# Performance work log

Hardware: AMD Instinct MI355X
Metric: run time of the kernel (lower is better)

## Reference

```python
import jax, jax.numpy as jnp
import numpy as np

N_NODES = 10000
N_EDGES = 500000
IN_DIM = 512
HID = 256
VOCAB = 1000


def _gat(x, src, dst, W, a_src, a_dst, b, n):
    # PyG GATConv, heads=1: linear, per-edge attention logits,
    # segment softmax over target node, scatter-weighted-sum.
    h = x @ W                              # [N, C]
    e = jax.nn.leaky_relu(jnp.take(h @ a_src, src) + jnp.take(h @ a_dst, dst), 0.2)  # [E]
    m = jax.ops.segment_max(e, dst, num_segments=n)
    w = jnp.exp(e - m[dst])
    denom = jax.ops.segment_sum(w, dst, num_segments=n)
    alpha = w / denom[dst]                 # [E]
    out = jax.ops.segment_sum(alpha[:, None] * h[src], dst, num_segments=n)  # [N, C]
    return out + b


def _lstm(seq, W_ih, W_hh, b_ih, b_hh):
    # torch nn.LSTM single layer, gate order i,f,g,o; batch of 1 -> scan over nodes
    H = W_hh.shape[1]
    pre = seq @ W_ih.T + (b_ih + b_hh)     # [T, 4H] precomputed input projection

    def step(carry, xt):
        h, c = carry
        g = xt + h @ W_hh.T
        i, f, gg, o = jnp.split(g, 4)
        i = jax.nn.sigmoid(i); f = jax.nn.sigmoid(f)
        gg = jnp.tanh(gg); o = jax.nn.sigmoid(o)
        c = f * c + i * gg
        h = o * jnp.tanh(c)
        return (h, c), h

    init = (jnp.zeros((H,), seq.dtype), jnp.zeros((H,), seq.dtype))
    _, hs = jax.lax.scan(step, init, pre)
    return hs                               # [T, H]


def setup_inputs() -> dict:
    key = jax.random.key(0)
    ks = jax.random.split(key, 16)
    s = 0.05
    x = jax.random.normal(ks[0], (N_NODES, IN_DIM), jnp.float32)
    edge_index = jax.random.randint(ks[1], (2, N_EDGES), 0, N_NODES, jnp.int32)
    return {
        "x": x,
        "W1": jax.random.normal(ks[2], (IN_DIM, HID), jnp.float32) * s,
        "a_src1": jax.random.normal(ks[3], (HID,), jnp.float32) * s,
        "a_dst1": jax.random.normal(ks[4], (HID,), jnp.float32) * s,
        "b1": jnp.zeros((HID,), jnp.float32),
        "W2": jax.random.normal(ks[5], (HID, HID), jnp.float32) * s,
        "a_src2": jax.random.normal(ks[6], (HID,), jnp.float32) * s,
        "a_dst2": jax.random.normal(ks[7], (HID,), jnp.float32) * s,
        "b2": jnp.zeros((HID,), jnp.float32),
        "W_ih": jax.random.normal(ks[8], (4 * HID, HID), jnp.float32) * s,
        "W_hh": jax.random.normal(ks[9], (4 * HID, HID), jnp.float32) * s,
        "b_ih": jnp.zeros((4 * HID,), jnp.float32),
        "b_hh": jnp.zeros((4 * HID,), jnp.float32),
        "Wfc": jax.random.normal(ks[10], (VOCAB, HID), jnp.float32) * s,
        "bfc": jnp.zeros((VOCAB,), jnp.float32),
        "edge_index": edge_index,
    }


def reference(x, W1, a_src1, a_dst1, b1, W2, a_src2, a_dst2, b2,
              W_ih, W_hh, b_ih, b_hh, Wfc, bfc, edge_index):
    n = x.shape[0]
    loops = jnp.arange(n, dtype=edge_index.dtype)
    src = jnp.concatenate([edge_index[0], loops])  # PyG adds self-loops
    dst = jnp.concatenate([edge_index[1], loops])
    h = jax.nn.relu(_gat(x, src, dst, W1, a_src1, a_dst1, b1, n))
    h = _gat(h, src, dst, W2, a_src2, a_dst2, b2, n)
    hs = _lstm(h, W_ih, W_hh, b_ih, b_hh)          # [N, HID]
    logits = hs @ Wfc.T + bfc                      # [N, VOCAB]
    return logits
```

## Files before the change

### kernel.cpp

```cpp
#include <hip/hip_runtime.h>
#include <cstdint>

#define N_NODES 10000
#define N_EDGES 500000
#define E_TOT   510000
#define IN_DIM  512
#define HID     256
#define VOCAB   1000

typedef _Float16 h2v __attribute__((ext_vector_type(2)));

__device__ __forceinline__ float fdot2f(h2v a, h2v b, float c) {
#if __has_builtin(__builtin_amdgcn_fdot2)
    return __builtin_amdgcn_fdot2(a, b, c, false);
#else
    return c + (float)a[0] * (float)b[0] + (float)a[1] * (float)b[1];
#endif
}

__device__ __forceinline__ float sigmoidf_(float x) {
    return 1.f / (1.f + __expf(-x));
}
__device__ __forceinline__ float tanhf_(float x) {
    float ax = fabsf(x);
    float e  = __expf(-2.f * ax);
    float r  = (1.f - e) / (1.f + e);
    return x < 0.f ? -r : r;
}

__device__ __forceinline__ unsigned uc4(const uint4& v, int j) {
    return j == 0 ? v.x : j == 1 ? v.y : j == 2 ? v.z : v.w;
}
__device__ __forceinline__ h2v bch(unsigned u) {
    return __builtin_bit_cast(h2v, u);
}
__device__ __forceinline__ h2v packf2(float2 v) {
    h2v w; w[0] = (_Float16)v.x; w[1] = (_Float16)v.y; return w;
}

template<bool TRANSB, int EPI>
__global__ __launch_bounds__(256) void gemm64(
    const float* __restrict__ A, const float* __restrict__ B,
    const float* __restrict__ bias, const float* __restrict__ bias2,
    float* __restrict__ C, int M, int N, int K, int ldc)
{
    __shared__ float As[16][68];
    __shared__ float Bs[16][68];
    const int tid = threadIdx.x;
    const int tx = tid & 15, ty = tid >> 4;
    const int m0 = blockIdx.x * 64, n0 = blockIdx.y * 64;
    float acc[4][4] = {};

    for (int k0 = 0; k0 < K; k0 += 16) {
        {
            int row = tid >> 2, col = (tid & 3) << 2;
            float4 v = make_float4(0.f, 0.f, 0.f, 0.f);
            if (m0 + row < M)
                v = *(const float4*)(A + (size_t)(m0 + row) * K + k0 + col);
            As[col + 0][row] = v.x; As[col + 1][row] = v.y;
            As[col + 2][row] = v.z; As[col + 3][row] = v.w;
        }
        if (!TRANSB) {
            int row = tid >> 4, col = (tid & 15) << 2;
            const float* bp = B + (size_t)(k0 + row) * N + n0 + col;
            float4 v = make_float4(0.f, 0.f, 0.f, 0.f);
            if (n0 + col + 3 < N) v = *(const float4*)bp;
            else {
                if (n0 + col + 0 < N) v.x = bp[0];
                if (n0 + col + 1 < N) v.y = bp[1];
                if (n0 + col + 2 < N) v.z = bp[2];
            }
            *(float4*)&Bs[row][col] = v;
        } else {
            int nr = tid >> 2, kc = (tid & 3) << 2;
            float4 v = make_float4(0.f, 0.f, 0.f, 0.f);
            if (n0 + nr < N)
                v = *(const float4*)(B + (size_t)(n0 + nr) * K + k0 + kc);
            Bs[kc + 0][nr] = v.x; Bs[kc + 1][nr] = v.y;
            Bs[kc + 2][nr] = v.z; Bs[kc + 3][nr] = v.w;
        }
        __syncthreads();
        #pragma unroll
        for (int kk = 0; kk < 16; ++kk) {
            float a[4], b[4];
            *(float4*)a = *(const float4*)&As[kk][ty << 2];
            *(float4*)b = *(const float4*)&Bs[kk][tx << 2];
            #pragma unroll
            for (int i = 0; i < 4; ++i)
                #pragma unroll
                for (int j = 0; j < 4; ++j)
                    acc[i][j] = fmaf(a[i], b[j], acc[i][j]);
        }
        __syncthreads();
    }
    #pragma unroll
    for (int i = 0; i < 4; ++i) {
        int m = m0 + (ty << 2) + i;
        if (m >= M) continue;
        #pragma unroll
        for (int j = 0; j < 4; ++j) {
            int n = n0 + (tx << 2) + j;
            if (n >= N) continue;
            float v = acc[i][j];
            if (bias)  v += bias[n];
            if (bias2) v += bias2[n];
            if (EPI == 1)
                C[(size_t)m * ldc + (((n & 255) << 2) + (n >> 8))] = v;
            else
                C[(size_t)m * ldc + n] = v;
        }
    }
}

__global__ __launch_bounds__(256) void scores_kernel(
    const float* __restrict__ H, const float* __restrict__ asrc,
    const float* __restrict__ adst, float* __restrict__ ssrc,
    float* __restrict__ sdst)
{
    int node = blockIdx.x * 4 + (threadIdx.x >> 6);
    int lane = threadIdx.x & 63;
    if (node >= N_NODES) return;
    float4 h = ((const float4*)H)[node * 64 + lane];
    float4 a = ((const float4*)asrc)[lane];
    float4 b = ((const float4*)adst)[lane];
    float ps = h.x * a.x + h.y * a.y + h.z * a.z + h.w * a.w;
    float pd = h.x * b.x + h.y * b.y + h.z * b.z + h.w * b.w;
    #pragma unroll
    for (int off = 32; off > 0; off >>= 1) {
        ps += __shfl_xor(ps, off);
        pd += __shfl_xor(pd, off);
    }
    if (lane == 0) { ssrc[node] = ps; sdst[node] = pd; }
}

__global__ __launch_bounds__(256) void edge_w_kernel(
    const int* __restrict__ ei, const float* __restrict__ ssrc,
    const float* __restrict__ sdst, float* __restrict__ wbuf,
    float* __restrict__ denom)
{
    int e = blockIdx.x * 256 + threadIdx.x;
    if (e >= E_TOT) return;
    int s, d;
    if (e < N_EDGES) { s = ei[e]; d = ei[N_EDGES + e]; }
    else             { s = d = e - N_EDGES; }
    float v = ssrc[s] + sdst[d];
    v = (v > 0.f) ? v : 0.2f * v;
    float w = __expf(v);
    wbuf[e] = w;
    unsafeAtomicAdd(&denom[d], w);
}

__global__ __launch_bounds__(256) void scatter_kernel(
    const int* __restrict__ ei, const float* __restrict__ H,
    const float* __restrict__ wbuf, float* __restrict__ S)
{
    int e = blockIdx.x * 4 + (threadIdx.x >> 6);
    int lane = threadIdx.x & 63;
    if (e >= E_TOT) return;
    int s, d;
    if (e < N_EDGES) { s = ei[e]; d = ei[N_EDGES + e]; }
    else             { s = d = e - N_EDGES; }
    float w = wbuf[e];
    float4 h = ((const float4*)H)[s * 64 + lane];
    float* outp = S + (size_t)d * HID + lane * 4;
    unsafeAtomicAdd(outp + 0, w * h.x);
    unsafeAtomicAdd(outp + 1, w * h.y);
    unsafeAtomicAdd(outp + 2, w * h.z);
    unsafeAtomicAdd(outp + 3, w * h.w);
}

__global__ __launch_bounds__(256) void finalize_kernel(
    const float* __restrict__ S, const float* __restrict__ denom,
    const float* __restrict__ bias, float* __restrict__ H, int relu)
{
    int idx = blockIdx.x * 256 + threadIdx.x;
    int n = idx >> 8, ci = idx & 255;
    float v = S[idx] / denom[n] + bias[ci];
    if (relu) v = fmaxf(v, 0.f);
    H[idx] = v;
}

__global__ __launch_bounds__(512, 2) void lstm_kernel(
    const float* __restrict__ Whh,
    const float* __restrict__ pre4,
    float* __restrict__ hs,
    uint4* __restrict__ oL2,
    int T)
{
    __shared__ uint4  oLds[512 * 8];
    __shared__ uint4  hsh[32];
    __shared__ float4 pf4[512];

    const int t  = threadIdx.x;
    const int r0 = t & 255, s = t >> 8;
    const int sw = t & 7;
    const int t8 = t * 8;

    h2v wi[64], wf[64], wg[64];
    {
        const float2* Wr = (const float2*)(Whh + (size_t)r0 * 256 + s * 128);
        #pragma unroll
        for (int j = 0; j < 64; ++j) wi[j] = packf2(Wr[j]);
        Wr = (const float2*)(Whh + (size_t)(r0 + 256) * 256 + s * 128);
        #pragma unroll
        for (int j = 0; j < 64; ++j) wf[j] = packf2(Wr[j]);
        Wr = (const float2*)(Whh + (size_t)(r0 + 512) * 256 + s * 128);
        #pragma unroll
        for (int j = 0; j < 64; ++j) wg[j] = packf2(Wr[j]);
        const float2* Wo = (const float2*)(Whh + (size_t)(r0 + 768) * 256 + s * 128);
        #pragma unroll
        for (int q = 0; q < 16; ++q) {
            unsigned dd[4];
            #pragma unroll
            for (int p = 0; p < 4; ++p)
                dd[p] = __builtin_bit_cast(unsigned, packf2(Wo[q * 4 + p]));
            uint4 pk = make_uint4(dd[0], dd[1], dd[2], dd[3]);
            if (q < 8) oLds[t8 + (q ^ sw)] = pk;
            else       oL2[(q - 8) * 512 + t] = pk;
        }
    }
    if (t < 32) hsh[t] = make_uint4(0, 0, 0, 0);
    float c = 0.f;
    float4 pren = make_float4(0.f, 0.f, 0.f, 0.f);
    if (t < 256) pren = ((const float4*)pre4)[t];
    __syncthreads();

    for (int step = 0; step < T; ++step) {
        float4 pnxt = pren;
        if (t < 256) {
            int ni = (step + 1 < T) ? (step + 1) : step;
            pnxt = ((const float4*)pre4)[(size_t)ni * 256 + t];
        }
        float ai, af, ag, ao;
        if (t < 256) { ai = pren.x; af = pren.y; ag = pren.z; ao = pren.w; }
        else         { ai = 0.f;    af = 0.f;    ag = 0.f;    ao = 0.f;    }

        #pragma unroll
        for (int ch = 0; ch < 8; ++ch) {
            uint4 ha = hsh[s * 16 + ch * 2 + 0];
            uint4 hb = hsh[s * 16 + ch * 2 + 1];
            uint4 oa, ob;
            if (ch < 4) {
                oa = oLds[t8 + ((2 * ch + 0) ^ sw)];
                ob = oLds[t8 + ((2 * ch + 1) ^ sw)];
            } else {
                oa = oL2[(size_t)(2 * ch - 8) * 512 + t];
                ob = oL2[(size_t)(2 * ch - 7) * 512 + t];
            }
            #pragma unroll
            for (int j = 0; j < 4; ++j) {
                h2v hh = bch(uc4(ha, j));
                ai = fdot2f(wi[ch * 8 + j], hh, ai);
                af = fdot2f(wf[ch * 8 + j], hh, af);
                ag = fdot2f(wg[ch * 8 + j], hh, ag);
                ao = fdot2f(bch(uc4(oa, j)), hh, ao);
            }
            #pragma unroll
            for (int j = 0; j < 4; ++j) {
                h2v hh = bch(uc4(hb, j));
                ai = fdot2f(wi[ch * 8 + 4 + j], hh, ai);
                af = fdot2f(wf[ch * 8 + 4 + j], hh, af);
                ag = fdot2f(wg[ch * 8 + 4 + j], hh, ag);
                ao = fdot2f(bch(uc4(ob, j)), hh, ao);
            }
        }
        pf4[t] = make_float4(ai, af, ag, ao);
        __syncthreads();
        if (t < 256) {
            float4 p0 = pf4[t], p1 = pf4[t + 256];
            float i_ = sigmoidf_(p0.x + p1.x);
            float f_ = sigmoidf_(p0.y + p1.y);
            float g_ = tanhf_(p0.z + p1.z);
            float o_ = sigmoidf_(p0.w + p1.w);
            c = fmaf(f_, c, i_ * g_);
            float hv = o_ * tanhf_(c);
            hs[(size_t)step * HID + t] = hv;
            ((_Float16*)hsh)[t] = (_Float16)hv;
            pren = pnxt;
        }
        __syncthreads();
    }
}

extern "C" void kernel_launch(void* const* d_in, const int* in_sizes, int n_in,
                              void* d_out, int out_size, void* d_ws, size_t ws_size,
                              hipStream_t stream)
{
    const float* x   = (const float*)d_in[0];
    const float* W1  = (const float*)d_in[1];
    const float* as1 = (const float*)d_in[2];
    const float* ad1 = (const float*)d_in[3];
    const float* b1  = (const float*)d_in[4];
    const float* W2  = (const float*)d_in[5];
    const float* as2 = (const float*)d_in[6];
    const float* ad2 = (const float*)d_in[7];
    const float* b2  = (const float*)d_in[8];
    const float* Wih = (const float*)d_in[9];
    const float* Whh = (const float*)d_in[10];
    const float* bih = (const float*)d_in[11];
    const float* bhh = (const float*)d_in[12];
    const float* Wfc = (const float*)d_in[13];
    const float* bfc = (const float*)d_in[14];
    const int*   ei  = (const int*)d_in[15];
    float* out = (float*)d_out;

    float* ws    = (float*)d_ws;
    float* A     = ws;
    float* Bsc   = ws +  2560000;
    float* Cbuf  = ws +  5120000;
    float* pre   = ws +  7680000;
    float* wbuf  = ws + 17920000;
    float* denom = ws + 18430000;
    float* ssrc  = ws + 18440000;
    float* sdst  = ws + 18450000;

    dim3 blk(256);

    gemm64<false, 0><<<dim3(157, 4), blk, 0, stream>>>(
        x, W1, nullptr, nullptr, A, N_NODES, HID, IN_DIM, HID);
    scores_kernel<<<2500, blk, 0, stream>>>(A, as1, ad1, ssrc, sdst);
    hipMemsetAsync(Bsc, 0, (size_t)N_NODES * HID * 4, stream);
    hipMemsetAsync(denom, 0, (size_t)N_NODES * 4, stream);
    edge_w_kernel<<<(E_TOT + 255) / 256, blk, 0, stream>>>(ei, ssrc, sdst, wbuf, denom);
    scatter_kernel<<<E_TOT / 4, blk, 0, stream>>>(ei, A, wbuf, Bsc);
    finalize_kernel<<<N_NODES, blk, 0, stream>>>(Bsc, denom, b1, Cbuf, 1);

    gemm64<false, 0><<<dim3(157, 4), blk, 0, stream>>>(
        Cbuf, W2, nullptr, nullptr, A, N_NODES, HID, HID, HID);
    scores_kernel<<<2500, blk, 0, stream>>>(A, as2, ad2, ssrc, sdst);
    hipMemsetAsync(Bsc, 0, (size_t)N_NODES * HID * 4, stream);
    hipMemsetAsync(denom, 0, (size_t)N_NODES * 4, stream);
    edge_w_kernel<<<(E_TOT + 255) / 256, blk, 0, stream>>>(ei, ssrc, sdst, wbuf, denom);
    scatter_kernel<<<E_TOT / 4, blk, 0, stream>>>(ei, A, wbuf, Bsc);
    finalize_kernel<<<N_NODES, blk, 0, stream>>>(Bsc, denom, b2, Cbuf, 0);

    gemm64<true, 1><<<dim3(157, 16), blk, 0, stream>>>(
        Cbuf, Wih, bih, bhh, pre, N_NODES, 4 * HID, HID, 4 * HID);
    lstm_kernel<<<1, 512, 0, stream>>>(Whh, pre, A, (uint4*)Bsc, N_NODES);

    gemm64<true, 0><<<dim3(157, 16), blk, 0, stream>>>(
        A, Wfc, bfc, nullptr, out, N_NODES, VOCAB, HID, VOCAB);
}
```

Measured before the change: 21.62 ms.

## Pair adjacent lanes per LSTM row, reduce via shuffle, double-buffer hidden state

Each LSTM hidden row is now split across two adjacent lanes, so the two partial sums are combined with a shuffle instead of an LDS exchange. This removes one of the two block barriers per timestep. The hidden state is double-buffered in LDS so the next step's h can be written without a second sync. The o-gate weights are redistributed: part stays in registers and the rest goes to LDS, which removes the global-memory (L2) spill of those weights at the cost of higher register pressure.

```diff
diff --git a/kernel.cpp b/kernel.cpp
--- a/kernel.cpp
+++ b/kernel.cpp
@@ -184,100 +184,85 @@
     const float* __restrict__ Whh,
     const float* __restrict__ pre4,
     float* __restrict__ hs,
-    uint4* __restrict__ oL2,
     int T)
 {
-    __shared__ uint4  oLds[512 * 8];
-    __shared__ uint4  hsh[32];
-    __shared__ float4 pf4[512];
+    __shared__ uint4 oT[12 * 512];
+    __shared__ uint4 hbuf[2][32];
 
     const int t  = threadIdx.x;
-    const int r0 = t & 255, s = t >> 8;
-    const int sw = t & 7;
-    const int t8 = t * 8;
-
-    h2v wi[64], wf[64], wg[64];
+    const int r  = t >> 1;
+    const int s  = t & 1;
+    const int hb = s << 4;
+
+    h2v wi[64], wf[64], wg[64], wo[16];
     {
-        const float2* Wr = (const float2*)(Whh + (size_t)r0 * 256 + s * 128);
+        const float2* Wr = (const float2*)(Whh + (size_t)r * 256 + s * 128);
         #pragma unroll
         for (int j = 0; j < 64; ++j) wi[j] = packf2(Wr[j]);
-        Wr = (const float2*)(Whh + (size_t)(r0 + 256) * 256 + s * 128);
+        Wr = (const float2*)(Whh + (size_t)(r + 256) * 256 + s * 128);
         #pragma unroll
         for (int j = 0; j < 64; ++j) wf[j] = packf2(Wr[j]);
-        Wr = (const float2*)(Whh + (size_t)(r0 + 512) * 256 + s * 128);
+        Wr = (const float2*)(Whh + (size_t)(r + 512) * 256 + s * 128);
         #pragma unroll
         for (int j = 0; j < 64; ++j) wg[j] = packf2(Wr[j]);
-        const float2* Wo = (const float2*)(Whh + (size_t)(r0 + 768) * 256 + s * 128);
-        #pragma unroll
-        for (int q = 0; q < 16; ++q) {
+        const float2* Wo = (const float2*)(Whh + (size_t)(r + 768) * 256 + s * 128);
+        #pragma unroll
+        for (int j = 0; j < 16; ++j) wo[j] = packf2(Wo[j]);
+        #pragma unroll
+        for (int k = 0; k < 12; ++k) {
             unsigned dd[4];
             #pragma unroll
             for (int p = 0; p < 4; ++p)
-                dd[p] = __builtin_bit_cast(unsigned, packf2(Wo[q * 4 + p]));
-            uint4 pk = make_uint4(dd[0], dd[1], dd[2], dd[3]);
-            if (q < 8) oLds[t8 + (q ^ sw)] = pk;
-            else       oL2[(q - 8) * 512 + t] = pk;
-        }
-    }
-    if (t < 32) hsh[t] = make_uint4(0, 0, 0, 0);
+                dd[p] = __builtin_bit_cast(unsigned, packf2(Wo[16 + k * 4 + p]));
+            oT[k * 512 + t] = make_uint4(dd[0], dd[1], dd[2], dd[3]);
+        }
+    }
+    if (t < 32) { hbuf[0][t] = make_uint4(0, 0, 0, 0); }
     float c = 0.f;
-    float4 pren = make_float4(0.f, 0.f, 0.f, 0.f);
-    if (t < 256) pren = ((const float4*)pre4)[t];
+    float4 pren = ((const float4*)pre4)[r];
     __syncthreads();
 
     for (int step = 0; step < T; ++step) {
-        float4 pnxt = pren;
-        if (t < 256) {
-            int ni = (step + 1 < T) ? (step + 1) : step;
-            pnxt = ((const float4*)pre4)[(size_t)ni * 256 + t];
-        }
+        const uint4* hcur = hbuf[step & 1];
+        uint4*       hnxt = hbuf[(step + 1) & 1];
+
+        int ni = (step + 1 < T) ? (step + 1) : step;
+        float4 pnxt = ((const float4*)pre4)[(size_t)ni * 256 + r];
+
         float ai, af, ag, ao;
-        if (t < 256) { ai = pren.x; af = pren.y; ag = pren.z; ao = pren.w; }
-        else         { ai = 0.f;    af = 0.f;    ag = 0.f;    ao = 0.f;    }
-
-        #pragma unroll
-        for (int ch = 0; ch < 8; ++ch) {
-            uint4 ha = hsh[s * 16 + ch * 2 + 0];
-            uint4 hb = hsh[s * 16 + ch * 2 + 1];
-            uint4 oa, ob;
-            if (ch < 4) {
-                oa = oLds[t8 + ((2 * ch + 0) ^ sw)];
-                ob = oLds[t8 + ((2 * ch + 1) ^ sw)];
-            } else {
-                oa = oL2[(size_t)(2 * ch - 8) * 512 + t];
-                ob = oL2[(size_t)(2 * ch - 7) * 512 + t];
-            }
+        if (s == 0) { ai = pren.x; af = pren.y; ag = pren.z; ao = pren.w; }
+        else        { ai = 0.f;    af = 0.f;    ag = 0.f;    ao = 0.f;    }
+
+        #pragma unroll
+        for (int k = 0; k < 16; ++k) {
+            uint4 hk = hcur[hb + k];
+            uint4 ok = (k < 4) ? __builtin_bit_cast(uint4, *(const h2v(*)[4])&wo[k * 4])
+                               : oT[(k - 4) * 512 + t];
             #pragma unroll
             for (int j = 0; j < 4; ++j) {
-                h2v hh = bch(uc4(ha, j));
-                ai = fdot2f(wi[ch * 8 + j], hh, ai);
-                af = fdot2f(wf[ch * 8 + j], hh, af);
-                ag = fdot2f(wg[ch * 8 + j], hh, ag);
-                ao = fdot2f(bch(uc4(oa, j)), hh, ao);
+                h2v hh = bch(uc4(hk, j));
+                ai = fdot2f(wi[k * 4 + j], hh, ai);
+                af = fdot2f(wf[k * 4 + j], hh, af);
+                ag = fdot2f(wg[k * 4 + j], hh, ag);
+                ao = fdot2f(bch(uc4(ok, j)), hh, ao);
             }
-            #pragma unroll
-            for (int j = 0; j < 4; ++j) {
-                h2v hh = bch(uc4(hb, j));
-                ai = fdot2f(wi[ch * 8 + 4 + j], hh, ai);
-                af = fdot2f(wf[ch * 8 + 4 + j], hh, af);
-                ag = fdot2f(wg[ch * 8 + 4 + j], hh, ag);
-                ao = fdot2f(bch(uc4(ob, j)), hh, ao);
-            }
-        }
-        pf4[t] = make_float4(ai, af, ag, ao);
-        __syncthreads();
-        if (t < 256) {
-            float4 p0 = pf4[t], p1 = pf4[t + 256];
-            float i_ = sigmoidf_(p0.x + p1.x);
-            float f_ = sigmoidf_(p0.y + p1.y);
-            float g_ = tanhf_(p0.z + p1.z);
-            float o_ = sigmoidf_(p0.w + p1.w);
-            c = fmaf(f_, c, i_ * g_);
-            float hv = o_ * tanhf_(c);
-            hs[(size_t)step * HID + t] = hv;
-            ((_Float16*)hsh)[t] = (_Float16)hv;
-            pren = pnxt;
-        }
+        }
+        ai += __shfl_xor(ai, 1);
+        af += __shfl_xor(af, 1);
+        ag += __shfl_xor(ag, 1);
+        ao += __shfl_xor(ao, 1);
+
+        float i_ = sigmoidf_(ai);
+        float f_ = sigmoidf_(af);
+        float g_ = tanhf_(ag);
+        float o_ = sigmoidf_(ao);
+        c = fmaf(f_, c, i_ * g_);
+        float hv = o_ * tanhf_(c);
+        if (s == 0) {
+            hs[(size_t)step * HID + r] = hv;
+            ((_Float16*)hnxt)[r] = (_Float16)hv;
+        }
+        pren = pnxt;
         __syncthreads();
     }
 }
@@ -336,7 +321,7 @@
 
     gemm64<true, 1><<<dim3(157, 16), blk, 0, stream>>>(
         Cbuf, Wih, bih, bhh, pre, N_NODES, 4 * HID, HID, 4 * HID);
-    lstm_kernel<<<1, 512, 0, stream>>>(Whh, pre, A, (uint4*)Bsc, N_NODES);
+    lstm_kernel<<<1, 512, 0, stream>>>(Whh, pre, A, N_NODES);
 
     gemm64<true, 0><<<dim3(157, 16), blk, 0, stream>>>(
         A, Wfc, bfc, nullptr, out, N_NODES, VOCAB, HID, VOCAB);
```

After: 20.43 ms. -5.5%, faster.
